# Kernel tuning notes

Hardware: AMD Instinct MI355X
Metric: run time of the kernel (lower is better)

Reference implementation:

```python
import jax, jax.numpy as jnp
import numpy as np


def setup_inputs() -> dict:
    key = jax.random.key(0)
    k1, k2 = jax.random.split(key)
    x = jax.random.normal(k1, (8, 8192, 128), dtype=jnp.float32)
    embed = jax.random.normal(k2, (1024, 128), dtype=jnp.float32)
    return {"x": x, "embed": embed}


def reference(x, embed):
    """EuclideanCodebook.forward, eval mode, c=0 (Euclidean path).

    x:     [..., D] inputs
    embed: [K, D] codebook
    Returns (quantize [..., D], embed_ind [...]).
    """
    shape = x.shape
    xf = x.reshape(-1, shape[-1])                      # (N, D)
    x2 = jnp.sum(xf * xf, axis=1, keepdims=True)       # (N, 1)
    e2 = jnp.sum(embed * embed, axis=1)                # (K,)
    dist = -(x2 - 2.0 * (xf @ embed.T) + e2[None, :])  # (N, K)
    embed_ind = jnp.argmax(dist, axis=-1)              # (N,)
    embed_ind = embed_ind.reshape(shape[:-1])          # postprocess_emb
    quantize = embed[embed_ind]                        # dequantize (gather)
    return quantize, embed_ind
```

## Files before the change

### kernel.cpp

```cpp
#include <hip/hip_runtime.h>

typedef _Float16 half8 __attribute__((ext_vector_type(8)));
typedef float f32x4 __attribute__((ext_vector_type(4)));

#define DD 128


__global__ void prep_frags_kernel(const float* __restrict__ embed,
                                  char* __restrict__ frag, int total) {
  int t = blockIdx.x * blockDim.x + threadIdx.x;
  if (t >= total) return;
  int lane = t & 63;
  int idx = (t >> 6) & 7;
  int c = t >> 9;
  int s = idx >> 1;
  int hl = idx & 1;
  int n = c * 16 + (lane & 15);
  int kb = s * 32 + ((lane >> 4) << 3);
  const float* src = embed + (size_t)n * DD + kb;
  _Float16* dst = (_Float16*)(frag + (size_t)c * 8192 + idx * 1024 + lane * 16);
#pragma unroll
  for (int j = 0; j < 8; ++j) {
    float v = src[j];
    _Float16 hi = (_Float16)v;
    dst[j] = hl ? (_Float16)(v - (float)hi) : hi;
  }
}

__global__ void prep_e2_kernel(const float* __restrict__ embed,
                               float* __restrict__ e2neg, int total) {
  int t = blockIdx.x * blockDim.x + threadIdx.x;
  if (t >= total) return;
  int lane = t & 63;
  int c = t >> 6;
  int n = c * 16 + (lane & 15);
  const float* src = embed + (size_t)n * DD;
  double s = 0.0;
  for (int j = 0; j < DD; ++j) { double v = (double)src[j]; s += v * v; }
  e2neg[c * 64 + lane] = (float)(-s);
}

__global__ __launch_bounds__(256) void vq_argmin_kernel(
    const float* __restrict__ x, const float* __restrict__ embed,
    const char* __restrict__ wsf, const float* __restrict__ wse,
    float* __restrict__ out_q, float* __restrict__ out_i, int nch) {
  const int lane = threadIdx.x & 63;
  const int w = threadIdx.x >> 6;
  const int m16 = lane & 15;
  const int g = lane >> 4;
  const int row0 = blockIdx.x * 128 + w * 32;

  half8 ah[2][4], al[2][4];
#pragma unroll
  for (int t = 0; t < 2; ++t) {
    const float* xrow = x + (size_t)(row0 + t * 16 + m16) * DD;
#pragma unroll
    for (int s = 0; s < 4; ++s) {
      const float* p = xrow + s * 32 + g * 8;
      f32x4 v0 = *(const f32x4*)(p);
      f32x4 v1 = *(const f32x4*)(p + 4);
#pragma unroll
      for (int j = 0; j < 4; ++j) {
        float v = v0[j];
        _Float16 hi = (_Float16)v;
        ah[t][s][j] = hi;
        al[t][s][j] = (_Float16)(v - (float)hi);
      }
#pragma unroll
      for (int j = 0; j < 4; ++j) {
        float v = v1[j];
        _Float16 hi = (_Float16)v;
        ah[t][s][4 + j] = hi;
        al[t][s][4 + j] = (_Float16)(v - (float)hi);
      }
    }
  }

  float bestv0[4], bestv1[4];
  int besti0[4], besti1[4];
#pragma unroll
  for (int r = 0; r < 4; ++r) {
    bestv0[r] = -__builtin_inff();
    bestv1[r] = -__builtin_inff();
    besti0[r] = 0;
    besti1[r] = 0;
  }

  half8 bhA[4], blA[4], bhB[4], blB[4];
  float neA, neB;

#define LOADB(BH, BL, NE, C)                                        \
  do {                                                              \
    const char* pf = wsf + (size_t)(C)*8192 + lane * 16;            \
    const char* pf1 = pf + 4096;                                    \
    BH[0] = *(const half8*)(pf);                                    \
    BL[0] = *(const half8*)(pf + 1024);                             \
    BH[1] = *(const half8*)(pf + 2048);                             \
    BL[1] = *(const half8*)(pf + 3072);                             \
    BH[2] = *(const half8*)(pf1);                                   \
    BL[2] = *(const half8*)(pf1 + 1024);                            \
    BH[3] = *(const half8*)(pf1 + 2048);                            \
    BL[3] = *(const half8*)(pf1 + 3072);                            \
    NE = wse[(size_t)(C)*64 + lane];                                \
  } while (0)

#define COMPUTE(BH, BL, NE, C)                                               \
  do {                                                                       \
    f32x4 acc0 = {0.f, 0.f, 0.f, 0.f};                                       \
    f32x4 acc1 = {0.f, 0.f, 0.f, 0.f};                                       \
    _Pragma("unroll") for (int s = 0; s < 4; ++s) {                          \
      acc0 = __builtin_amdgcn_mfma_f32_16x16x32_f16(ah[0][s], BH[s], acc0,   \
                                                    0, 0, 0);                \
      acc1 = __builtin_amdgcn_mfma_f32_16x16x32_f16(ah[1][s], BH[s], acc1,   \
                                                    0, 0, 0);                \
      acc0 = __builtin_amdgcn_mfma_f32_16x16x32_f16(al[0][s], BH[s], acc0,   \
                                                    0, 0, 0);                \
      acc1 = __builtin_amdgcn_mfma_f32_16x16x32_f16(al[1][s], BH[s], acc1,   \
                                                    0, 0, 0);                \
      acc0 = __builtin_amdgcn_mfma_f32_16x16x32_f16(ah[0][s], BL[s], acc0,   \
                                                    0, 0, 0);                \
      acc1 = __builtin_amdgcn_mfma_f32_16x16x32_f16(ah[1][s], BL[s], acc1,   \
                                                    0, 0, 0);                \
    }                                                                        \
    const int n_ = (C)*16 + m16;                                             \
    _Pragma("unroll") for (int r = 0; r < 4; ++r) {                          \
      float s0 = fmaf(2.f, acc0[r], NE);                                     \
      if (s0 > bestv0[r]) { bestv0[r] = s0; besti0[r] = n_; }                \
      float s1 = fmaf(2.f, acc1[r], NE);                                     \
      if (s1 > bestv1[r]) { bestv1[r] = s1; besti1[r] = n_; }                \
    }                                                                        \
  } while (0)

  LOADB(bhA, blA, neA, 0);
  for (int c = 0; c < nch; c += 2) {
    LOADB(bhB, blB, neB, c + 1);
    COMPUTE(bhA, blA, neA, c);
    if (c + 2 < nch) LOADB(bhA, blA, neA, c + 2);
    COMPUTE(bhB, blB, neB, c + 1);
  }
#undef LOADB
#undef COMPUTE

#pragma unroll
  for (int off = 1; off < 16; off <<= 1) {
#pragma unroll
    for (int r = 0; r < 4; ++r) {
      float ov0 = __shfl_xor(bestv0[r], off, 64);
      int oi0 = __shfl_xor(besti0[r], off, 64);
      if (ov0 > bestv0[r] || (ov0 == bestv0[r] && oi0 < besti0[r])) {
        bestv0[r] = ov0;
        besti0[r] = oi0;
      }
      float ov1 = __shfl_xor(bestv1[r], off, 64);
      int oi1 = __shfl_xor(besti1[r], off, 64);
      if (ov1 > bestv1[r] || (ov1 == bestv1[r] && oi1 < besti1[r])) {
        bestv1[r] = ov1;
        besti1[r] = oi1;
      }
    }
  }

#pragma unroll
  for (int t = 0; t < 2; ++t) {
#pragma unroll
    for (int r = 0; r < 4; ++r) {
      const int row = row0 + t * 16 + g * 4 + r;
      const int idx = t ? besti1[r] : besti0[r];
      if (m16 == 0) out_i[row] = (float)idx;
      const f32x4* src = (const f32x4*)(embed + (size_t)idx * DD) + m16 * 2;
      f32x4* dst = (f32x4*)(out_q + (size_t)row * DD) + m16 * 2;
      dst[0] = src[0];
      dst[1] = src[1];
    }
  }
}

__global__ void vq_fallback_kernel(const float* __restrict__ x,
                                   const float* __restrict__ embed,
                                   float* __restrict__ out_q,
                                   float* __restrict__ out_i, int N, int K) {
  int row = blockIdx.x * blockDim.x + threadIdx.x;
  if (row >= N) return;
  const float* xr = x + (size_t)row * DD;
  float xv[DD];
  for (int j = 0; j < DD; ++j) xv[j] = xr[j];
  double best = -1e300;
  int bi = 0;
  for (int k = 0; k < K; ++k) {
    const float* e = embed + (size_t)k * DD;
    double acc = 0.0;
    for (int j = 0; j < DD; ++j) {
      double d = (double)xv[j] - (double)e[j];
      acc += d * d;
    }
    double sc = -acc;
    if (sc > best) { best = sc; bi = k; }
  }
  out_i[row] = (float)bi;
  for (int j = 0; j < DD; ++j)
    out_q[(size_t)row * DD + j] = embed[(size_t)bi * DD + j];
}

extern "C" void kernel_launch(void* const* d_in, const int* in_sizes, int n_in,
                              void* d_out, int out_size, void* d_ws,
                              size_t ws_size, hipStream_t stream) {
  const float* x = (const float*)d_in[0];
  const float* embed = (const float*)d_in[1];
  const int N = in_sizes[0] / DD;
  const int K = in_sizes[1] / DD;
  float* out_q = (float*)d_out;
  float* out_i = out_q + (size_t)N * DD;

  const int nch = K / 16;
  const size_t frag_bytes = (size_t)nch * 8192;
  const size_t e2_bytes = (size_t)nch * 256;
  const size_t need = frag_bytes + e2_bytes;

  if (ws_size < need || (N % 128) != 0 || (K % 16) != 0) {
    vq_fallback_kernel<<<(N + 255) / 256, 256, 0, stream>>>(x, embed, out_q,
                                                            out_i, N, K);
    return;
  }

  char* wsf = (char*)d_ws;
  float* wse = (float*)(wsf + frag_bytes);

  const int total_f = nch * 8 * 64;
  prep_frags_kernel<<<(total_f + 255) / 256, 256, 0, stream>>>(embed, wsf,
                                                               total_f);
  const int total_e = nch * 64;
  prep_e2_kernel<<<(total_e + 255) / 256, 256, 0, stream>>>(embed, wse,
                                                            total_e);
  vq_argmin_kernel<<<N / 128, 256, 0, stream>>>(x, embed, wsf, wse, out_q,
                                                out_i, nch);
}
```

Measured before the change: 70.37 us.

## Warp-specialize argmin: MFMA waves write scores to LDS, extra waves reduce

Adds two extra waves per block that run the argmax over MFMA results staged in double-buffered, swizzled LDS, while four waves keep issuing MFMAs, pipelined with block barriers. It also merges the two prep kernels into one launch and rewrites the final gather to use all threads with 128 rows per block. The aim is to take the compare/select epilogue off the MFMA waves and save a launch. The cost is two __syncthreads per chunk pair and LDS traffic, plus new fallback constraints on nch.

```diff
diff --git a/kernel.cpp b/kernel.cpp
--- a/kernel.cpp
+++ b/kernel.cpp
@@ -6,8 +6,9 @@
 #define DD 128
 
 
-__global__ void prep_frags_kernel(const float* __restrict__ embed,
-                                  char* __restrict__ frag, int total) {
+__global__ void prep_kernel(const float* __restrict__ embed,
+                            char* __restrict__ frag,
+                            float* __restrict__ e2neg, int total) {
   int t = blockIdx.x * blockDim.x + threadIdx.x;
   if (t >= total) return;
   int lane = t & 63;
@@ -25,71 +26,41 @@
     _Float16 hi = (_Float16)v;
     dst[j] = hl ? (_Float16)(v - (float)hi) : hi;
   }
-}
-
-__global__ void prep_e2_kernel(const float* __restrict__ embed,
-                               float* __restrict__ e2neg, int total) {
-  int t = blockIdx.x * blockDim.x + threadIdx.x;
-  if (t >= total) return;
-  int lane = t & 63;
-  int c = t >> 6;
-  int n = c * 16 + (lane & 15);
-  const float* src = embed + (size_t)n * DD;
-  double s = 0.0;
-  for (int j = 0; j < DD; ++j) { double v = (double)src[j]; s += v * v; }
-  e2neg[c * 64 + lane] = (float)(-s);
-}
-
-__global__ __launch_bounds__(256) void vq_argmin_kernel(
+  if (idx == 0) {
+    const float* e = embed + (size_t)n * DD;
+    double acc = 0.0;
+    for (int j = 0; j < DD; ++j) { double v = (double)e[j]; acc += v * v; }
+    e2neg[c * 64 + lane] = (float)(-acc);
+  }
+}
+
+__global__ __launch_bounds__(384) void vq_argmin_kernel(
     const float* __restrict__ x, const float* __restrict__ embed,
     const char* __restrict__ wsf, const float* __restrict__ wse,
     float* __restrict__ out_q, float* __restrict__ out_i, int nch) {
-  const int lane = threadIdx.x & 63;
-  const int w = threadIdx.x >> 6;
+  const int tid = threadIdx.x;
+  const int lane = tid & 63;
+  const int w = tid >> 6;
   const int m16 = lane & 15;
   const int g = lane >> 4;
-  const int row0 = blockIdx.x * 128 + w * 32;
+  const int blk_row0 = blockIdx.x * 128;
+
+  __shared__ alignas(16) char sbuf[2][8192];
+  __shared__ float lds_e2[1024];
+  __shared__ int idxbuf[128];
+
+  for (int i = tid; i < nch * 16; i += 384)
+    lds_e2[i] = wse[(size_t)(i >> 4) * 64 + (i & 15)];
 
   half8 ah[2][4], al[2][4];
-#pragma unroll
-  for (int t = 0; t < 2; ++t) {
-    const float* xrow = x + (size_t)(row0 + t * 16 + m16) * DD;
-#pragma unroll
-    for (int s = 0; s < 4; ++s) {
-      const float* p = xrow + s * 32 + g * 8;
-      f32x4 v0 = *(const f32x4*)(p);
-      f32x4 v1 = *(const f32x4*)(p + 4);
-#pragma unroll
-      for (int j = 0; j < 4; ++j) {
-        float v = v0[j];
-        _Float16 hi = (_Float16)v;
-        ah[t][s][j] = hi;
-        al[t][s][j] = (_Float16)(v - (float)hi);
-      }
-#pragma unroll
-      for (int j = 0; j < 4; ++j) {
-        float v = v1[j];
-        _Float16 hi = (_Float16)v;
-        ah[t][s][4 + j] = hi;
-        al[t][s][4 + j] = (_Float16)(v - (float)hi);
-      }
-    }
-  }
-
-  float bestv0[4], bestv1[4];
-  int besti0[4], besti1[4];
-#pragma unroll
-  for (int r = 0; r < 4; ++r) {
-    bestv0[r] = -__builtin_inff();
-    bestv1[r] = -__builtin_inff();
-    besti0[r] = 0;
-    besti1[r] = 0;
-  }
-
   half8 bhA[4], blA[4], bhB[4], blB[4];
-  float neA, neB;
-
-#define LOADB(BH, BL, NE, C)                                        \
+  const int crow = ((w & 1) << 6) | lane;
+  const int rb_hi = (crow << 2) & 0x1F0;
+  const int rb_lo = (crow << 2) & 12;
+  float bestv = -__builtin_inff();
+  int besti = 0;
+
+#define LOADB(BH, BL, C)                                            \
   do {                                                              \
     const char* pf = wsf + (size_t)(C)*8192 + lane * 16;            \
     const char* pf1 = pf + 4096;                                    \
@@ -101,10 +72,9 @@
     BL[2] = *(const half8*)(pf1 + 1024);                            \
     BH[3] = *(const half8*)(pf1 + 2048);                            \
     BL[3] = *(const half8*)(pf1 + 3072);                            \
-    NE = wse[(size_t)(C)*64 + lane];                                \
   } while (0)
 
-#define COMPUTE(BH, BL, NE, C)                                               \
+#define COMPUTE(BH, BL, BUF)                                                 \
   do {                                                                       \
     f32x4 acc0 = {0.f, 0.f, 0.f, 0.f};                                       \
     f32x4 acc1 = {0.f, 0.f, 0.f, 0.f};                                       \
@@ -122,56 +92,87 @@
       acc1 = __builtin_amdgcn_mfma_f32_16x16x32_f16(ah[1][s], BL[s], acc1,   \
                                                     0, 0, 0);                \
     }                                                                        \
-    const int n_ = (C)*16 + m16;                                             \
-    _Pragma("unroll") for (int r = 0; r < 4; ++r) {                          \
-      float s0 = fmaf(2.f, acc0[r], NE);                                     \
-      if (s0 > bestv0[r]) { bestv0[r] = s0; besti0[r] = n_; }                \
-      float s1 = fmaf(2.f, acc1[r], NE);                                     \
-      if (s1 > bestv1[r]) { bestv1[r] = s1; besti1[r] = n_; }                \
+    const int lr0_ = (w << 5) + (g << 2);                                    \
+    const int lr1_ = lr0_ + 16;                                              \
+    char* sb_ = &sbuf[BUF][m16 << 9];                                        \
+    *(f32x4*)(sb_ + ((lr0_ << 2) ^ (m16 << 4))) = acc0;                      \
+    *(f32x4*)(sb_ + ((lr1_ << 2) ^ (m16 << 4))) = acc1;                      \
+  } while (0)
+
+#define ARGMAX(CC)                                                           \
+  do {                                                                       \
+    const int cc_ = (CC);                                                    \
+    const char* sb_ = &sbuf[cc_ & 1][0];                                     \
+    _Pragma("unroll") for (int k = 0; k < 16; ++k) {                         \
+      float sv = *(const float*)(sb_ + (k << 9) + ((rb_hi ^ (k << 4)) | rb_lo)); \
+      float sc = fmaf(2.f, sv, lds_e2[cc_ * 16 + k]);                        \
+      if (sc > bestv) { bestv = sc; besti = cc_ * 16 + k; }                  \
     }                                                                        \
   } while (0)
 
-  LOADB(bhA, blA, neA, 0);
+  if (w < 4) {
+    const int row0 = blk_row0 + w * 32;
+#pragma unroll
+    for (int t = 0; t < 2; ++t) {
+      const float* xrow = x + (size_t)(row0 + t * 16 + m16) * DD;
+#pragma unroll
+      for (int s = 0; s < 4; ++s) {
+        const float* p = xrow + s * 32 + g * 8;
+        f32x4 v0 = *(const f32x4*)(p);
+        f32x4 v1 = *(const f32x4*)(p + 4);
+#pragma unroll
+        for (int j = 0; j < 4; ++j) {
+          float v = v0[j];
+          _Float16 hi = (_Float16)v;
+          ah[t][s][j] = hi;
+          al[t][s][j] = (_Float16)(v - (float)hi);
+        }
+#pragma unroll
+        for (int j = 0; j < 4; ++j) {
+          float v = v1[j];
+          _Float16 hi = (_Float16)v;
+          ah[t][s][4 + j] = hi;
+          al[t][s][4 + j] = (_Float16)(v - (float)hi);
+        }
+      }
+    }
+    LOADB(bhA, blA, 0);
+  }
+  __syncthreads();
+
   for (int c = 0; c < nch; c += 2) {
-    LOADB(bhB, blB, neB, c + 1);
-    COMPUTE(bhA, blA, neA, c);
-    if (c + 2 < nch) LOADB(bhA, blA, neA, c + 2);
-    COMPUTE(bhB, blB, neB, c + 1);
+    if (w < 4) {
+      LOADB(bhB, blB, c + 1);
+      COMPUTE(bhA, blA, 0);
+    } else if (c) {
+      ARGMAX(c - 1);
+    }
+    __syncthreads();
+    if (w < 4) {
+      if (c + 2 < nch) LOADB(bhA, blA, c + 2);
+      COMPUTE(bhB, blB, 1);
+    } else {
+      ARGMAX(c);
+    }
+    __syncthreads();
   }
 #undef LOADB
 #undef COMPUTE
 
-#pragma unroll
-  for (int off = 1; off < 16; off <<= 1) {
-#pragma unroll
-    for (int r = 0; r < 4; ++r) {
-      float ov0 = __shfl_xor(bestv0[r], off, 64);
-      int oi0 = __shfl_xor(besti0[r], off, 64);
-      if (ov0 > bestv0[r] || (ov0 == bestv0[r] && oi0 < besti0[r])) {
-        bestv0[r] = ov0;
-        besti0[r] = oi0;
-      }
-      float ov1 = __shfl_xor(bestv1[r], off, 64);
-      int oi1 = __shfl_xor(besti1[r], off, 64);
-      if (ov1 > bestv1[r] || (ov1 == bestv1[r] && oi1 < besti1[r])) {
-        bestv1[r] = ov1;
-        besti1[r] = oi1;
-      }
-    }
-  }
-
-#pragma unroll
-  for (int t = 0; t < 2; ++t) {
-#pragma unroll
-    for (int r = 0; r < 4; ++r) {
-      const int row = row0 + t * 16 + g * 4 + r;
-      const int idx = t ? besti1[r] : besti0[r];
-      if (m16 == 0) out_i[row] = (float)idx;
-      const f32x4* src = (const f32x4*)(embed + (size_t)idx * DD) + m16 * 2;
-      f32x4* dst = (f32x4*)(out_q + (size_t)row * DD) + m16 * 2;
-      dst[0] = src[0];
-      dst[1] = src[1];
-    }
+  if (w >= 4) {
+    ARGMAX(nch - 1);
+    idxbuf[crow] = besti;
+  }
+#undef ARGMAX
+  __syncthreads();
+
+  if (tid < 128) out_i[blk_row0 + tid] = (float)idxbuf[tid];
+  const int hw = tid >> 5;
+  const int l32 = tid & 31;
+  for (int r = hw; r < 128; r += 12) {
+    const int idx = idxbuf[r];
+    f32x4 v = *((const f32x4*)(embed + (size_t)idx * DD) + l32);
+    *((f32x4*)(out_q + (size_t)(blk_row0 + r) * DD) + l32) = v;
   }
 }
 
@@ -216,7 +217,8 @@
   const size_t e2_bytes = (size_t)nch * 256;
   const size_t need = frag_bytes + e2_bytes;
 
-  if (ws_size < need || (N % 128) != 0 || (K % 16) != 0) {
+  if (ws_size < need || (N % 128) != 0 || (K % 16) != 0 || (nch % 2) != 0 ||
+      nch < 2 || nch > 64) {
     vq_fallback_kernel<<<(N + 255) / 256, 256, 0, stream>>>(x, embed, out_q,
                                                             out_i, N, K);
     return;
@@ -226,11 +228,8 @@
   float* wse = (float*)(wsf + frag_bytes);
 
   const int total_f = nch * 8 * 64;
-  prep_frags_kernel<<<(total_f + 255) / 256, 256, 0, stream>>>(embed, wsf,
-                                                               total_f);
-  const int total_e = nch * 64;
-  prep_e2_kernel<<<(total_e + 255) / 256, 256, 0, stream>>>(embed, wse,
-                                                            total_e);
-  vq_argmin_kernel<<<N / 128, 256, 0, stream>>>(x, embed, wsf, wse, out_q,
+  prep_kernel<<<(total_f + 255) / 256, 256, 0, stream>>>(embed, wsf, wse,
+                                                         total_f);
+  vq_argmin_kernel<<<N / 128, 384, 0, stream>>>(x, embed, wsf, wse, out_q,
                                                 out_i, nch);
 }
```

New measurement: 100.4 us. +42.6%, slower.

## Software-pipeline MFMA and argmax epilogue across chunks; merge prep kernels

Applied to the files above, without the earlier changes.

Restructures the main loop into a four-stage rotation in which each codebook chunk's MFMA results are consumed two chunks later, so the argmax epilogue overlaps with later MFMAs instead of waiting on MFMA latency. It also folds the squared-norm prep into the fragment prep kernel, saving one launch. In exchange it holds more accumulator registers live, which may cut occupancy, and it adds a guard that sends codebooks whose chunk count is not a multiple of four to the fallback path.

```diff
diff --git a/kernel.cpp b/kernel.cpp
--- a/kernel.cpp
+++ b/kernel.cpp
@@ -6,8 +6,9 @@
 #define DD 128
 
 
-__global__ void prep_frags_kernel(const float* __restrict__ embed,
-                                  char* __restrict__ frag, int total) {
+__global__ void prep_kernel(const float* __restrict__ embed,
+                            char* __restrict__ frag,
+                            float* __restrict__ e2neg, int total) {
   int t = blockIdx.x * blockDim.x + threadIdx.x;
   if (t >= total) return;
   int lane = t & 63;
@@ -25,19 +26,12 @@
     _Float16 hi = (_Float16)v;
     dst[j] = hl ? (_Float16)(v - (float)hi) : hi;
   }
-}
-
-__global__ void prep_e2_kernel(const float* __restrict__ embed,
-                               float* __restrict__ e2neg, int total) {
-  int t = blockIdx.x * blockDim.x + threadIdx.x;
-  if (t >= total) return;
-  int lane = t & 63;
-  int c = t >> 6;
-  int n = c * 16 + (lane & 15);
-  const float* src = embed + (size_t)n * DD;
-  double s = 0.0;
-  for (int j = 0; j < DD; ++j) { double v = (double)src[j]; s += v * v; }
-  e2neg[c * 64 + lane] = (float)(-s);
+  if (idx == 0) {
+    const float* e = embed + (size_t)n * DD;
+    double acc = 0.0;
+    for (int j = 0; j < DD; ++j) { double v = (double)e[j]; acc += v * v; }
+    e2neg[c * 64 + lane] = (float)(-acc);
+  }
 }
 
 __global__ __launch_bounds__(256) void vq_argmin_kernel(
@@ -87,7 +81,8 @@
   }
 
   half8 bhA[4], blA[4], bhB[4], blB[4];
-  float neA, neB;
+  float ne0, ne1, ne2, ne3;
+  f32x4 p0a, p0b, p1a, p1b, p2a, p2b, p3a, p3b;
 
 #define LOADB(BH, BL, NE, C)                                        \
   do {                                                              \
@@ -104,42 +99,68 @@
     NE = wse[(size_t)(C)*64 + lane];                                \
   } while (0)
 
-#define COMPUTE(BH, BL, NE, C)                                               \
+#define MFMA_CHUNK(ACC0, ACC1, BH, BL)                                       \
   do {                                                                       \
-    f32x4 acc0 = {0.f, 0.f, 0.f, 0.f};                                       \
-    f32x4 acc1 = {0.f, 0.f, 0.f, 0.f};                                       \
+    ACC0 = f32x4{0.f, 0.f, 0.f, 0.f};                                        \
+    ACC1 = f32x4{0.f, 0.f, 0.f, 0.f};                                        \
     _Pragma("unroll") for (int s = 0; s < 4; ++s) {                          \
-      acc0 = __builtin_amdgcn_mfma_f32_16x16x32_f16(ah[0][s], BH[s], acc0,   \
-                                                    0, 0, 0);                \
-      acc1 = __builtin_amdgcn_mfma_f32_16x16x32_f16(ah[1][s], BH[s], acc1,   \
-                                                    0, 0, 0);                \
-      acc0 = __builtin_amdgcn_mfma_f32_16x16x32_f16(al[0][s], BH[s], acc0,   \
-                                                    0, 0, 0);                \
-      acc1 = __builtin_amdgcn_mfma_f32_16x16x32_f16(al[1][s], BH[s], acc1,   \
-                                                    0, 0, 0);                \
-      acc0 = __builtin_amdgcn_mfma_f32_16x16x32_f16(ah[0][s], BL[s], acc0,   \
-                                                    0, 0, 0);                \
-      acc1 = __builtin_amdgcn_mfma_f32_16x16x32_f16(ah[1][s], BL[s], acc1,   \
+      ACC0 = __builtin_amdgcn_mfma_f32_16x16x32_f16(ah[0][s], BH[s], ACC0,   \
+                                                    0, 0, 0);                \
+      ACC1 = __builtin_amdgcn_mfma_f32_16x16x32_f16(ah[1][s], BH[s], ACC1,   \
+                                                    0, 0, 0);                \
+      ACC0 = __builtin_amdgcn_mfma_f32_16x16x32_f16(al[0][s], BH[s], ACC0,   \
+                                                    0, 0, 0);                \
+      ACC1 = __builtin_amdgcn_mfma_f32_16x16x32_f16(al[1][s], BH[s], ACC1,   \
+                                                    0, 0, 0);                \
+      ACC0 = __builtin_amdgcn_mfma_f32_16x16x32_f16(ah[0][s], BL[s], ACC0,   \
+                                                    0, 0, 0);                \
+      ACC1 = __builtin_amdgcn_mfma_f32_16x16x32_f16(ah[1][s], BL[s], ACC1,   \
                                                     0, 0, 0);                \
     }                                                                        \
+  } while (0)
+
+#define EPI(ACC0, ACC1, NE, C)                                               \
+  do {                                                                       \
     const int n_ = (C)*16 + m16;                                             \
     _Pragma("unroll") for (int r = 0; r < 4; ++r) {                          \
-      float s0 = fmaf(2.f, acc0[r], NE);                                     \
+      float s0 = fmaf(2.f, ACC0[r], NE);                                     \
       if (s0 > bestv0[r]) { bestv0[r] = s0; besti0[r] = n_; }                \
-      float s1 = fmaf(2.f, acc1[r], NE);                                     \
+      float s1 = fmaf(2.f, ACC1[r], NE);                                     \
       if (s1 > bestv1[r]) { bestv1[r] = s1; besti1[r] = n_; }                \
     }                                                                        \
   } while (0)
 
-  LOADB(bhA, blA, neA, 0);
-  for (int c = 0; c < nch; c += 2) {
-    LOADB(bhB, blB, neB, c + 1);
-    COMPUTE(bhA, blA, neA, c);
-    if (c + 2 < nch) LOADB(bhA, blA, neA, c + 2);
-    COMPUTE(bhB, blB, neB, c + 1);
-  }
+  LOADB(bhA, blA, ne0, 0);
+  LOADB(bhB, blB, ne1, 1);
+  MFMA_CHUNK(p0a, p0b, bhA, blA);
+  LOADB(bhA, blA, ne2, 2);
+  MFMA_CHUNK(p1a, p1b, bhB, blB);
+  LOADB(bhB, blB, ne3, 3);
+  MFMA_CHUNK(p2a, p2b, bhA, blA);
+  EPI(p0a, p0b, ne0, 0);
+  if (4 < nch) LOADB(bhA, blA, ne0, 4);
+  MFMA_CHUNK(p3a, p3b, bhB, blB);
+  EPI(p1a, p1b, ne1, 1);
+
+  for (int c = 4; c < nch; c += 4) {
+    LOADB(bhB, blB, ne1, c + 1);
+    MFMA_CHUNK(p0a, p0b, bhA, blA);
+    EPI(p2a, p2b, ne2, c - 2);
+    LOADB(bhA, blA, ne2, c + 2);
+    MFMA_CHUNK(p1a, p1b, bhB, blB);
+    EPI(p3a, p3b, ne3, c - 1);
+    LOADB(bhB, blB, ne3, c + 3);
+    MFMA_CHUNK(p2a, p2b, bhA, blA);
+    EPI(p0a, p0b, ne0, c);
+    if (c + 4 < nch) LOADB(bhA, blA, ne0, c + 4);
+    MFMA_CHUNK(p3a, p3b, bhB, blB);
+    EPI(p1a, p1b, ne1, c + 1);
+  }
+  EPI(p2a, p2b, ne2, nch - 2);
+  EPI(p3a, p3b, ne3, nch - 1);
 #undef LOADB
-#undef COMPUTE
+#undef MFMA_CHUNK
+#undef EPI
 
 #pragma unroll
   for (int off = 1; off < 16; off <<= 1) {
@@ -216,7 +237,8 @@
   const size_t e2_bytes = (size_t)nch * 256;
   const size_t need = frag_bytes + e2_bytes;
 
-  if (ws_size < need || (N % 128) != 0 || (K % 16) != 0) {
+  if (ws_size < need || (N % 128) != 0 || (K % 16) != 0 || (nch % 4) != 0 ||
+      nch < 8) {
     vq_fallback_kernel<<<(N + 255) / 256, 256, 0, stream>>>(x, embed, out_q,
                                                             out_i, N, K);
     return;
@@ -226,11 +248,8 @@
   float* wse = (float*)(wsf + frag_bytes);
 
   const int total_f = nch * 8 * 64;
-  prep_frags_kernel<<<(total_f + 255) / 256, 256, 0, stream>>>(embed, wsf,
-                                                               total_f);
-  const int total_e = nch * 64;
-  prep_e2_kernel<<<(total_e + 255) / 256, 256, 0, stream>>>(embed, wse,
-                                                            total_e);
+  prep_kernel<<<(total_f + 255) / 256, 256, 0, stream>>>(embed, wsf, wse,
+                                                         total_f);
   vq_argmin_kernel<<<N / 128, 256, 0, stream>>>(x, embed, wsf, wse, out_q,
                                                 out_i, nch);
 }
```

New measurement: 65.28 us. -7.2%, faster.
